# Performance work log

Measured on AMD Instinct MI355X. Metric: run time of the kernel, lower is better.

The kernel has to match this reference:

```python
import jax, jax.numpy as jnp
import numpy as np

B, N, F_IN, F_OUT, H = 8, 1024, 128, 64, 4
EPS = 1e-7
NEG_SLOPE = 0.2


def setup_inputs() -> dict:
    key = jax.random.key(0)
    k_a, k_x, k_w, k_aw, k_ab = jax.random.split(key, 5)
    A = jax.random.randint(k_a, (B, N, N), 0, 2).astype(jnp.float32)
    x = jax.random.normal(k_x, (B, N, F_IN), dtype=jnp.float32)
    # per-head params (stacked over head axis): GAT.W (xavier-normal-ish), attention Linear(2F->1)
    W = jax.random.normal(k_w, (H, F_IN, F_OUT), dtype=jnp.float32) * np.sqrt(2.0 / (F_IN + F_OUT))
    lim = 1.0 / np.sqrt(2 * F_OUT)
    a_w = jax.random.uniform(k_aw, (H, 2 * F_OUT), minval=-lim, maxval=lim, dtype=jnp.float32)
    a_b = jax.random.uniform(k_ab, (H,), minval=-lim, maxval=lim, dtype=jnp.float32)
    return {"A": A, "x": x, "W": W, "a_w": a_w, "a_b": a_b}


def reference(A, x, W, a_w, a_b):
    # Wh: (B, H, N, F_OUT)
    Wh = jnp.einsum('bnf,hfo->bhno', x, W)
    # attention linear on concat([Wh_i, Wh_j]) is separable: a1.Wh_i + a2.Wh_j + b
    a1, a2 = a_w[:, :F_OUT], a_w[:, F_OUT:]
    s_i = jnp.einsum('bhno,ho->bhn', Wh, a1)   # depends on row index i (dim 1 of (B,N,N))
    s_j = jnp.einsum('bhno,ho->bhn', Wh, a2)   # depends on col index j (dim 2)
    e = s_i[:, :, :, None] + s_j[:, :, None, :] + a_b[None, :, None, None]  # (B,H,Ni,Nj)
    e = jnp.where(e >= 0, e, NEG_SLOPE * e)  # LeakyReLU(0.2)
    # masked softmax as in source: exp, mask by A, normalize over dim=1 of (B,N,N) -> axis 2 here
    exps = jnp.exp(e) * A[:, None, :, :]
    attn = exps / (jnp.sum(exps, axis=2, keepdims=True) + EPS)
    out = jnp.einsum('bhij,bhjo->bhio', attn, Wh)  # matmul over j
    # concat heads on feature dim: (B, N, H*F_OUT)
    return out.transpose(0, 2, 1, 3).reshape(B, N, H * F_OUT)
```

## Files before the change

### kernel.cpp

```cpp
#include <hip/hip_runtime.h>
#include <hip/hip_bf16.h>
#include <hip/hip_fp16.h>

#define BB 8
#define NN 1024
#define FIN 128
#define FOUT 64
#define HH 4
#define EPSV 1e-7f
#define SLOPE 0.2f
#define LOG2E 1.44269504088896340736f

typedef _Float16 v8h __attribute__((ext_vector_type(8)));
typedef _Float16 v4h __attribute__((ext_vector_type(4)));
typedef float v4f __attribute__((ext_vector_type(4)));

__global__ __launch_bounds__(256) void k0_wt(const float* __restrict__ W,
                                             _Float16* __restrict__ Wtt) {
  for (int it = 0; it < 16; ++it) {
    int idx = blockIdx.x * 4096 + it * 256 + threadIdx.x;
    int e = idx & 7, ln = (idx >> 3) & 15, kgg = (idx >> 7) & 15,
        ct = idx >> 11;
    int c = ct * 16 + ln, k = kgg * 8 + e;
    Wtt[idx] = (_Float16)W[(size_t)(c >> 6) * 8192 + k * 64 + (c & 63)];
  }
}

__global__ __launch_bounds__(256) void k1_whm(const float* __restrict__ x,
                                              const _Float16* __restrict__ Wtt,
                                              const float* __restrict__ aw,
                                              const float* __restrict__ ab,
                                              _Float16* __restrict__ WhH,
                                              float* __restrict__ si2,
                                              float* __restrict__ tj2) {
  __shared__ _Float16 xs[16][136];
  int tid = threadIdx.x;
#pragma unroll
  for (int t2 = 0; t2 < 2; ++t2) {
    int idx = t2 * 256 + tid;
    int row = idx >> 5, c4 = (idx & 31) * 4;
    float4 v = *(const float4*)(x + ((size_t)blockIdx.x * 16 + row) * FIN + c4);
    v4h hv;
    hv[0] = (_Float16)v.x; hv[1] = (_Float16)v.y;
    hv[2] = (_Float16)v.z; hv[3] = (_Float16)v.w;
    *(v4h*)(&xs[row][c4]) = hv;
  }
  __syncthreads();
  int w = tid >> 6, l = tid & 63;
  int kg = l >> 4, ln = l & 15;
  v4f acc[4] = {{}, {}, {}, {}};
#pragma unroll
  for (int ks = 0; ks < 4; ++ks) {
    v8h af = *(const v8h*)(&xs[ln][ks * 32 + kg * 8]);
    int kgg = ks * 4 + kg;
#pragma unroll
    for (int t = 0; t < 4; ++t) {
      int ct = w * 4 + t;
      v8h bf = *(const v8h*)(Wtt + (((size_t)ct * 16 + kgg) * 16 + ln) * 8);
      acc[t] = __builtin_amdgcn_mfma_f32_16x16x32_f16(af, bf, acc[t], 0, 0, 0);
    }
  }
  float a1v[4], a2v[4];
#pragma unroll
  for (int t = 0; t < 4; ++t) {
    a1v[t] = aw[w * 128 + t * 16 + ln];
    a2v[t] = aw[w * 128 + 64 + t * 16 + ln];
  }
  float abv = ab[w];
#pragma unroll
  for (int r = 0; r < 4; ++r) {
    float v1 = acc[0][r] * a1v[0] + acc[1][r] * a1v[1] +
               acc[2][r] * a1v[2] + acc[3][r] * a1v[3];
    float v2 = acc[0][r] * a2v[0] + acc[1][r] * a2v[1] +
               acc[2][r] * a2v[2] + acc[3][r] * a2v[3];
#pragma unroll
    for (int off = 1; off < 16; off <<= 1) {
      v1 += __shfl_xor(v1, off);
      v2 += __shfl_xor(v2, off);
    }
    if (ln == 0) {
      int gr = blockIdx.x * 16 + kg * 4 + r;
      int b_ = gr >> 10, n_ = gr & 1023;
      size_t row = ((size_t)b_ * HH + w) * NN + n_;
      si2[row] = v1 * LOG2E;
      tj2[row] = (v2 + abv) * LOG2E;
    }
  }
#pragma unroll
  for (int t = 0; t < 4; ++t) {
#pragma unroll
    for (int r = 0; r < 4; ++r) {
      int gr = blockIdx.x * 16 + kg * 4 + r;
      int b_ = gr >> 10, n_ = gr & 1023;
      WhH[(((size_t)b_ * HH + w) * NN + n_) * 64 + (t * 16 + ln)] =
          (_Float16)acc[t][r];
    }
  }
}

__global__ __launch_bounds__(256) void kb_colsum_bits(
    const float* __restrict__ A, const float* __restrict__ si2,
    const float* __restrict__ tj2, float* __restrict__ part,
    unsigned long long* __restrict__ Abits) {
  __shared__ float sil[4][32];
  int b = blockIdx.z, is = blockIdx.y, jt = blockIdx.x;
  int tid = threadIdx.x;
  int w = tid >> 6, lane = tid & 63;
  int j = jt * 256 + tid;
  int i0 = is * 32;
  if (tid < 128) {
    int h = tid >> 5, ii = tid & 31;
    sil[h][ii] = si2[((size_t)(b * HH + h)) * NN + i0 + ii];
  }
  __syncthreads();
  float tjv[4], acc[4] = {0.f, 0.f, 0.f, 0.f};
#pragma unroll
  for (int h = 0; h < 4; ++h) tjv[h] = tj2[((size_t)(b * HH + h)) * NN + j];
  const float* Ap = A + ((size_t)b * NN + i0) * NN + j;
  unsigned long long myword = 0ull;
#pragma unroll
  for (int c = 0; c < 4; ++c) {
    float av[8];
#pragma unroll
    for (int q = 0; q < 8; ++q)
      av[q] = Ap[(size_t)(c * 8 + q) * NN];
#pragma unroll
    for (int q = 0; q < 8; ++q) {
      unsigned long long m = __ballot(av[q] != 0.0f);
      if (lane == c * 8 + q) myword = m;
      int ii = c * 8 + q;
#pragma unroll
      for (int h = 0; h < 4; ++h) {
        float f = sil[h][ii] + tjv[h];
        float g = fmaxf(f, SLOPE * f);
        acc[h] += av[q] * __builtin_amdgcn_exp2f(g);
      }
    }
  }
  if (lane < 32)
    Abits[((size_t)b * NN + i0 + lane) * 16 + jt * 4 + w] = myword;
#pragma unroll
  for (int h = 0; h < 4; ++h)
    part[((size_t)(is * 32) + b * HH + h) * NN + j] = acc[h];
}

__global__ __launch_bounds__(256) void k3_scale_tr(
    const _Float16* __restrict__ WhH, const float* __restrict__ part,
    _Float16* __restrict__ VTt) {
  __shared__ float rbuf[64];
  __shared__ _Float16 tile[64 * 66];
  int bid = blockIdx.x;
  int b = bid & 7, rest = bid >> 3;
  int h = rest & 3, jt = rest >> 2;
  int bh = b * HH + h, j0 = jt * 64;
  int tid = threadIdx.x;
  if (tid < 64) {
    float s = 0.f;
#pragma unroll
    for (int is = 0; is < 32; ++is)
      s += part[((size_t)(is * 32) + bh) * NN + j0 + tid];
    rbuf[tid] = 1.0f / (s + EPSV);
  }
  __syncthreads();
#pragma unroll
  for (int it = 0; it < 16; ++it) {
    int lin = it * 256 + tid;
    int jj = lin >> 6, o = lin & 63;
    float v = (float)WhH[((size_t)bh * NN + j0 + jj) * 64 + o] * rbuf[jj];
    tile[o * 66 + jj] = (_Float16)v;
  }
  __syncthreads();
#pragma unroll
  for (int it = 0; it < 16; ++it) {
    int lin = it * 256 + tid;
    int o = lin >> 6, jj64 = lin & 63;
    int j = j0 + jj64;
    int jb = j >> 5, jj = j & 31;
    VTt[(((size_t)bh * 32 + jb) * 64 + o) * 32 + jj] = tile[o * 66 + jj64];
  }
}

__global__ __launch_bounds__(512) void k4_pv(
    const unsigned long long* __restrict__ Abits,
    const float* __restrict__ si2, const float* __restrict__ tj2,
    const _Float16* __restrict__ VTt, float* __restrict__ out) {
  __shared__ unsigned long long Ab[32][17];
  __shared__ float tjl[4][1024];
  __shared__ float sil[4][32];
  __shared__ float red[4][64][33];
  int bid = blockIdx.x;
  int b = bid & 7, it = bid >> 3;
  int i0 = it * 32;
  int tid = threadIdx.x;
#pragma unroll
  for (int t2 = 0; t2 < 8; ++t2) {
    int idx = t2 * 512 + tid;
    int h = idx >> 10, j = idx & 1023;
    tjl[h][j] = tj2[((size_t)(b * HH + h)) * NN + j];
  }
  if (tid < 128) {
    int h = tid >> 5, ii = tid & 31;
    sil[h][ii] = si2[((size_t)(b * HH + h)) * NN + i0 + ii];
  }
  {
    int row = tid >> 4, word = tid & 15;
    Ab[row][word] = Abits[((size_t)b * NN + i0 + row) * 16 + word];
  }
  __syncthreads();

  int w = tid >> 6, l = tid & 63;
  int h = w & 3, jh = w >> 2;
  int kg = l >> 4, ln = l & 15;
  float si0 = sil[h][ln];
  float si1 = sil[h][16 + ln];
  int bh = b * HH + h;
  v4f acc0[4] = {{}, {}, {}, {}};
  v4f acc1[4] = {{}, {}, {}, {}};
  const _Float16* VTb = VTt + (size_t)bh * 32 * 64 * 32;
  const float* tj = tjl[h];
  int jbase = jh * 512;

#define PEXP(si, tv) \
  __builtin_amdgcn_exp2f(fmaxf((si) + (tv), SLOPE * ((si) + (tv))))

#pragma unroll 2
  for (int jq = 0; jq < 16; ++jq) {
    int j = jbase + jq * 32 + kg * 8;
    int widx = j >> 6, sh = j & 63;
    unsigned int bits0 = (unsigned int)(Ab[ln][widx] >> sh) & 0xffu;
    unsigned int bits1 = (unsigned int)(Ab[16 + ln][widx] >> sh) & 0xffu;
    float4 t0 = *(const float4*)(tj + j);
    float4 t1 = *(const float4*)(tj + j + 4);
    v8h af0, af1;
    af0[0] = (bits0 & 1u) ? (_Float16)PEXP(si0, t0.x) : (_Float16)0;
    af0[1] = (bits0 & 2u) ? (_Float16)PEXP(si0, t0.y) : (_Float16)0;
    af0[2] = (bits0 & 4u) ? (_Float16)PEXP(si0, t0.z) : (_Float16)0;
    af0[3] = (bits0 & 8u) ? (_Float16)PEXP(si0, t0.w) : (_Float16)0;
    af0[4] = (bits0 & 16u) ? (_Float16)PEXP(si0, t1.x) : (_Float16)0;
    af0[5] = (bits0 & 32u) ? (_Float16)PEXP(si0, t1.y) : (_Float16)0;
    af0[6] = (bits0 & 64u) ? (_Float16)PEXP(si0, t1.z) : (_Float16)0;
    af0[7] = (bits0 & 128u) ? (_Float16)PEXP(si0, t1.w) : (_Float16)0;
    af1[0] = (bits1 & 1u) ? (_Float16)PEXP(si1, t0.x) : (_Float16)0;
    af1[1] = (bits1 & 2u) ? (_Float16)PEXP(si1, t0.y) : (_Float16)0;
    af1[2] = (bits1 & 4u) ? (_Float16)PEXP(si1, t0.z) : (_Float16)0;
    af1[3] = (bits1 & 8u) ? (_Float16)PEXP(si1, t0.w) : (_Float16)0;
    af1[4] = (bits1 & 16u) ? (_Float16)PEXP(si1, t1.x) : (_Float16)0;
    af1[5] = (bits1 & 32u) ? (_Float16)PEXP(si1, t1.y) : (_Float16)0;
    af1[6] = (bits1 & 64u) ? (_Float16)PEXP(si1, t1.z) : (_Float16)0;
    af1[7] = (bits1 & 128u) ? (_Float16)PEXP(si1, t1.w) : (_Float16)0;
    const _Float16* vb = VTb + (size_t)(j >> 5) * 2048 + kg * 8;
    v8h b0 = *(const v8h*)(vb + (0 * 16 + ln) * 32);
    v8h b1 = *(const v8h*)(vb + (1 * 16 + ln) * 32);
    v8h b2 = *(const v8h*)(vb + (2 * 16 + ln) * 32);
    v8h b3 = *(const v8h*)(vb + (3 * 16 + ln) * 32);
    acc0[0] = __builtin_amdgcn_mfma_f32_16x16x32_f16(af0, b0, acc0[0], 0, 0, 0);
    acc1[0] = __builtin_amdgcn_mfma_f32_16x16x32_f16(af1, b0, acc1[0], 0, 0, 0);
    acc0[1] = __builtin_amdgcn_mfma_f32_16x16x32_f16(af0, b1, acc0[1], 0, 0, 0);
    acc1[1] = __builtin_amdgcn_mfma_f32_16x16x32_f16(af1, b1, acc1[1], 0, 0, 0);
    acc0[2] = __builtin_amdgcn_mfma_f32_16x16x32_f16(af0, b2, acc0[2], 0, 0, 0);
    acc1[2] = __builtin_amdgcn_mfma_f32_16x16x32_f16(af1, b2, acc1[2], 0, 0, 0);
    acc0[3] = __builtin_amdgcn_mfma_f32_16x16x32_f16(af0, b3, acc0[3], 0, 0, 0);
    acc1[3] = __builtin_amdgcn_mfma_f32_16x16x32_f16(af1, b3, acc1[3], 0, 0, 0);
  }
#undef PEXP

  if (jh) {
#pragma unroll
    for (int t = 0; t < 4; ++t)
#pragma unroll
      for (int r = 0; r < 4; ++r) {
        red[h][l][t * 4 + r] = acc0[t][r];
        red[h][l][16 + t * 4 + r] = acc1[t][r];
      }
  }
  __syncthreads();
  if (!jh) {
#pragma unroll
    for (int t = 0; t < 4; ++t)
#pragma unroll
      for (int r = 0; r < 4; ++r) {
        acc0[t][r] += red[h][l][t * 4 + r];
        acc1[t][r] += red[h][l][16 + t * 4 + r];
      }
#pragma unroll
    for (int r = 0; r < 4; ++r) {
      int gi0 = i0 + kg * 4 + r;
      float* op0 = out + ((size_t)b * NN + gi0) * 256 + h * 64;
      op0[0 * 16 + ln] = acc0[0][r];
      op0[1 * 16 + ln] = acc0[1][r];
      op0[2 * 16 + ln] = acc0[2][r];
      op0[3 * 16 + ln] = acc0[3][r];
      float* op1 = op0 + 16 * 256;
      op1[0 * 16 + ln] = acc1[0][r];
      op1[1 * 16 + ln] = acc1[1][r];
      op1[2 * 16 + ln] = acc1[2][r];
      op1[3 * 16 + ln] = acc1[3][r];
    }
  }
}

extern "C" void kernel_launch(void* const* d_in, const int* in_sizes, int n_in,
                              void* d_out, int out_size, void* d_ws,
                              size_t ws_size, hipStream_t stream) {
  const float* A = (const float*)d_in[0];
  const float* x = (const float*)d_in[1];
  const float* W = (const float*)d_in[2];
  const float* aw = (const float*)d_in[3];
  const float* ab = (const float*)d_in[4];
  float* out = (float*)d_out;
  char* ws = (char*)d_ws;
  _Float16* WhH = (_Float16*)ws;
  _Float16* VTt = (_Float16*)(ws + (4u << 20));
  _Float16* Wtt = (_Float16*)(ws + (8u << 20));
  float* si2 = (float*)(ws + (8u << 20) + (256u << 10));
  float* tj2 = (float*)(ws + (8u << 20) + (384u << 10));
  float* part = (float*)(ws + (8u << 20) + (512u << 10));
  unsigned long long* Abits =
      (unsigned long long*)(ws + (12u << 20) + (512u << 10));

  hipLaunchKernelGGL(k0_wt, dim3(8), dim3(256), 0, stream, W, Wtt);
  hipLaunchKernelGGL(k1_whm, dim3(512), dim3(256), 0, stream, x, Wtt, aw, ab,
                     WhH, si2, tj2);
  hipLaunchKernelGGL(kb_colsum_bits, dim3(4, 32, BB), dim3(256), 0, stream, A,
                     si2, tj2, part, Abits);
  hipLaunchKernelGGL(k3_scale_tr, dim3(512), dim3(256), 0, stream, WhH, part,
                     VTt);
  hipLaunchKernelGGL(k4_pv, dim3(256), dim3(512), 0, stream, Abits, si2, tj2,
                     VTt, out);
}
```

Baseline: 49.62 us.

## Split k4_pv heads across blocks with 4-way j split and packed fp16 conversion

The PV kernel now gives each block two heads instead of four and splits the j range four ways across waves. This doubles the grid to 512 blocks and cuts per-block shared memory, raising occupancy via launch_bounds(512,4). The four partial sums are combined with a two-stage shared-memory tree, which adds syncthreads. The per-element fp16 casts become packed cvt_pkrtz, which rounds toward zero instead of to nearest, and each block now re-reads the adjacency bits even though it covers only two heads.

```diff
diff --git a/kernel.cpp b/kernel.cpp
--- a/kernel.cpp
+++ b/kernel.cpp
@@ -13,6 +13,7 @@
 
 typedef _Float16 v8h __attribute__((ext_vector_type(8)));
 typedef _Float16 v4h __attribute__((ext_vector_type(4)));
+typedef __fp16 v2hf __attribute__((ext_vector_type(2)));
 typedef float v4f __attribute__((ext_vector_type(4)));
 
 __global__ __launch_bounds__(256) void k0_wt(const float* __restrict__ W,
@@ -180,74 +181,81 @@
   }
 }
 
-__global__ __launch_bounds__(512) void k4_pv(
+__global__ __launch_bounds__(512, 4) void k4_pv(
     const unsigned long long* __restrict__ Abits,
     const float* __restrict__ si2, const float* __restrict__ tj2,
     const _Float16* __restrict__ VTt, float* __restrict__ out) {
   __shared__ unsigned long long Ab[32][17];
-  __shared__ float tjl[4][1024];
-  __shared__ float sil[4][32];
-  __shared__ float red[4][64][33];
+  __shared__ float tjl[2][1024];
+  __shared__ float sil[2][32];
+  __shared__ float red[2][2][64][32];
   int bid = blockIdx.x;
-  int b = bid & 7, it = bid >> 3;
+  int b = bid & 7, hp = (bid >> 3) & 1, it = bid >> 4;
   int i0 = it * 32;
   int tid = threadIdx.x;
 #pragma unroll
-  for (int t2 = 0; t2 < 8; ++t2) {
+  for (int t2 = 0; t2 < 4; ++t2) {
     int idx = t2 * 512 + tid;
-    int h = idx >> 10, j = idx & 1023;
-    tjl[h][j] = tj2[((size_t)(b * HH + h)) * NN + j];
-  }
-  if (tid < 128) {
-    int h = tid >> 5, ii = tid & 31;
-    sil[h][ii] = si2[((size_t)(b * HH + h)) * NN + i0 + ii];
+    int hh = idx >> 10, j = idx & 1023;
+    tjl[hh][j] = tj2[((size_t)(b * HH + hp * 2 + hh)) * NN + j];
+  }
+  if (tid < 64) {
+    int hh = tid >> 5, ii = tid & 31;
+    sil[hh][ii] = si2[((size_t)(b * HH + hp * 2 + hh)) * NN + i0 + ii];
   }
   {
     int row = tid >> 4, word = tid & 15;
-    Ab[row][word] = Abits[((size_t)b * NN + i0 + row) * 16 + word];
+    if (word < 16) Ab[row][word] = Abits[((size_t)b * NN + i0 + row) * 16 + word];
   }
   __syncthreads();
 
   int w = tid >> 6, l = tid & 63;
-  int h = w & 3, jh = w >> 2;
+  int hh = w & 1, jq4 = w >> 1;
   int kg = l >> 4, ln = l & 15;
-  float si0 = sil[h][ln];
-  float si1 = sil[h][16 + ln];
-  int bh = b * HH + h;
+  float si0 = sil[hh][ln];
+  float si1 = sil[hh][16 + ln];
+  int bh = b * HH + hp * 2 + hh;
   v4f acc0[4] = {{}, {}, {}, {}};
   v4f acc1[4] = {{}, {}, {}, {}};
   const _Float16* VTb = VTt + (size_t)bh * 32 * 64 * 32;
-  const float* tj = tjl[h];
-  int jbase = jh * 512;
+  const float* tj = tjl[hh];
+  int jbase = jq4 * 256;
 
 #define PEXP(si, tv) \
   __builtin_amdgcn_exp2f(fmaxf((si) + (tv), SLOPE * ((si) + (tv))))
 
 #pragma unroll 2
-  for (int jq = 0; jq < 16; ++jq) {
+  for (int jq = 0; jq < 8; ++jq) {
     int j = jbase + jq * 32 + kg * 8;
     int widx = j >> 6, sh = j & 63;
     unsigned int bits0 = (unsigned int)(Ab[ln][widx] >> sh) & 0xffu;
     unsigned int bits1 = (unsigned int)(Ab[16 + ln][widx] >> sh) & 0xffu;
     float4 t0 = *(const float4*)(tj + j);
     float4 t1 = *(const float4*)(tj + j + 4);
-    v8h af0, af1;
-    af0[0] = (bits0 & 1u) ? (_Float16)PEXP(si0, t0.x) : (_Float16)0;
-    af0[1] = (bits0 & 2u) ? (_Float16)PEXP(si0, t0.y) : (_Float16)0;
-    af0[2] = (bits0 & 4u) ? (_Float16)PEXP(si0, t0.z) : (_Float16)0;
-    af0[3] = (bits0 & 8u) ? (_Float16)PEXP(si0, t0.w) : (_Float16)0;
-    af0[4] = (bits0 & 16u) ? (_Float16)PEXP(si0, t1.x) : (_Float16)0;
-    af0[5] = (bits0 & 32u) ? (_Float16)PEXP(si0, t1.y) : (_Float16)0;
-    af0[6] = (bits0 & 64u) ? (_Float16)PEXP(si0, t1.z) : (_Float16)0;
-    af0[7] = (bits0 & 128u) ? (_Float16)PEXP(si0, t1.w) : (_Float16)0;
-    af1[0] = (bits1 & 1u) ? (_Float16)PEXP(si1, t0.x) : (_Float16)0;
-    af1[1] = (bits1 & 2u) ? (_Float16)PEXP(si1, t0.y) : (_Float16)0;
-    af1[2] = (bits1 & 4u) ? (_Float16)PEXP(si1, t0.z) : (_Float16)0;
-    af1[3] = (bits1 & 8u) ? (_Float16)PEXP(si1, t0.w) : (_Float16)0;
-    af1[4] = (bits1 & 16u) ? (_Float16)PEXP(si1, t1.x) : (_Float16)0;
-    af1[5] = (bits1 & 32u) ? (_Float16)PEXP(si1, t1.y) : (_Float16)0;
-    af1[6] = (bits1 & 64u) ? (_Float16)PEXP(si1, t1.z) : (_Float16)0;
-    af1[7] = (bits1 & 128u) ? (_Float16)PEXP(si1, t1.w) : (_Float16)0;
+    float p0[8], p1[8];
+    p0[0] = (bits0 & 1u) ? PEXP(si0, t0.x) : 0.f;
+    p0[1] = (bits0 & 2u) ? PEXP(si0, t0.y) : 0.f;
+    p0[2] = (bits0 & 4u) ? PEXP(si0, t0.z) : 0.f;
+    p0[3] = (bits0 & 8u) ? PEXP(si0, t0.w) : 0.f;
+    p0[4] = (bits0 & 16u) ? PEXP(si0, t1.x) : 0.f;
+    p0[5] = (bits0 & 32u) ? PEXP(si0, t1.y) : 0.f;
+    p0[6] = (bits0 & 64u) ? PEXP(si0, t1.z) : 0.f;
+    p0[7] = (bits0 & 128u) ? PEXP(si0, t1.w) : 0.f;
+    p1[0] = (bits1 & 1u) ? PEXP(si1, t0.x) : 0.f;
+    p1[1] = (bits1 & 2u) ? PEXP(si1, t0.y) : 0.f;
+    p1[2] = (bits1 & 4u) ? PEXP(si1, t0.z) : 0.f;
+    p1[3] = (bits1 & 8u) ? PEXP(si1, t0.w) : 0.f;
+    p1[4] = (bits1 & 16u) ? PEXP(si1, t1.x) : 0.f;
+    p1[5] = (bits1 & 32u) ? PEXP(si1, t1.y) : 0.f;
+    p1[6] = (bits1 & 64u) ? PEXP(si1, t1.z) : 0.f;
+    p1[7] = (bits1 & 128u) ? PEXP(si1, t1.w) : 0.f;
+    union { v2hf h2[4]; v8h h8; } u0, u1;
+#pragma unroll
+    for (int q = 0; q < 4; ++q) {
+      u0.h2[q] = __builtin_amdgcn_cvt_pkrtz(p0[2 * q], p0[2 * q + 1]);
+      u1.h2[q] = __builtin_amdgcn_cvt_pkrtz(p1[2 * q], p1[2 * q + 1]);
+    }
+    v8h af0 = u0.h8, af1 = u1.h8;
     const _Float16* vb = VTb + (size_t)(j >> 5) * 2048 + kg * 8;
     v8h b0 = *(const v8h*)(vb + (0 * 16 + ln) * 32);
     v8h b1 = *(const v8h*)(vb + (1 * 16 + ln) * 32);
@@ -264,28 +272,50 @@
   }
 #undef PEXP
 
-  if (jh) {
+  if (jq4 == 1 || jq4 == 3) {
+    int slot = jq4 >> 1;
 #pragma unroll
     for (int t = 0; t < 4; ++t)
 #pragma unroll
       for (int r = 0; r < 4; ++r) {
-        red[h][l][t * 4 + r] = acc0[t][r];
-        red[h][l][16 + t * 4 + r] = acc1[t][r];
-      }
-  }
-  __syncthreads();
-  if (!jh) {
+        red[hh][slot][l][t * 4 + r] = acc0[t][r];
+        red[hh][slot][l][16 + t * 4 + r] = acc1[t][r];
+      }
+  }
+  __syncthreads();
+  if (jq4 == 0 || jq4 == 2) {
+    int slot = jq4 >> 1;
 #pragma unroll
     for (int t = 0; t < 4; ++t)
 #pragma unroll
       for (int r = 0; r < 4; ++r) {
-        acc0[t][r] += red[h][l][t * 4 + r];
-        acc1[t][r] += red[h][l][16 + t * 4 + r];
+        acc0[t][r] += red[hh][slot][l][t * 4 + r];
+        acc1[t][r] += red[hh][slot][l][16 + t * 4 + r];
+      }
+  }
+  __syncthreads();
+  if (jq4 == 2) {
+#pragma unroll
+    for (int t = 0; t < 4; ++t)
+#pragma unroll
+      for (int r = 0; r < 4; ++r) {
+        red[hh][0][l][t * 4 + r] = acc0[t][r];
+        red[hh][0][l][16 + t * 4 + r] = acc1[t][r];
+      }
+  }
+  __syncthreads();
+  if (jq4 == 0) {
+#pragma unroll
+    for (int t = 0; t < 4; ++t)
+#pragma unroll
+      for (int r = 0; r < 4; ++r) {
+        acc0[t][r] += red[hh][0][l][t * 4 + r];
+        acc1[t][r] += red[hh][0][l][16 + t * 4 + r];
       }
 #pragma unroll
     for (int r = 0; r < 4; ++r) {
       int gi0 = i0 + kg * 4 + r;
-      float* op0 = out + ((size_t)b * NN + gi0) * 256 + h * 64;
+      float* op0 = out + ((size_t)b * NN + gi0) * 256 + (hp * 2 + hh) * 64;
       op0[0 * 16 + ln] = acc0[0][r];
       op0[1 * 16 + ln] = acc0[1][r];
       op0[2 * 16 + ln] = acc0[2][r];
@@ -325,6 +355,6 @@
                      si2, tj2, part, Abits);
   hipLaunchKernelGGL(k3_scale_tr, dim3(512), dim3(256), 0, stream, WhH, part,
                      VTt);
-  hipLaunchKernelGGL(k4_pv, dim3(256), dim3(512), 0, stream, Abits, si2, tj2,
+  hipLaunchKernelGGL(k4_pv, dim3(512), dim3(512), 0, stream, Abits, si2, tj2,
                      VTt, out);
 }
```

Result: faster. 48.60 us (-2.1%).
